# Optimization experiments

Hardware: AMD Instinct MI355X
Metric: run time of the kernel (lower is better)

Reference implementation:

```python
import jax, jax.numpy as jnp
import numpy as np

B, S, D, H = 2, 2048, 1024, 16
ND = D // H  # head dim = 64


def setup_inputs() -> dict:
    key = jax.random.key(0)
    ks = jax.random.split(key, 11)
    scale = 1.0 / np.sqrt(D)
    inp = {
        "q": jax.random.normal(ks[0], (B, S, D), dtype=jnp.float32),
        "k": jax.random.normal(ks[1], (B, S, D), dtype=jnp.float32),
        "v": jax.random.normal(ks[2], (B, S, D), dtype=jnp.float32),
        # causal mask, broadcast over batch and heads
        "mask": jnp.tril(jnp.ones((S, S), dtype=jnp.int32))[None, None, :, :],
        "Wq": jax.random.normal(ks[3], (D, D), dtype=jnp.float32) * scale,
        "bq": jnp.zeros((D,), dtype=jnp.float32),
        "Wk": jax.random.normal(ks[4], (D, D), dtype=jnp.float32) * scale,
        "bk": jnp.zeros((D,), dtype=jnp.float32),
        "Wv": jax.random.normal(ks[5], (D, D), dtype=jnp.float32) * scale,
        "bv": jnp.zeros((D,), dtype=jnp.float32),
        "Wo": jax.random.normal(ks[6], (D, D), dtype=jnp.float32) * scale,
        "bo": jnp.zeros((D,), dtype=jnp.float32),
    }
    return inp


def reference(q, k, v, mask, Wq, bq, Wk, bk, Wv, bv, Wo, bo):
    batch, seq_len, _ = q.shape
    # torch nn.Linear: x @ W.T + b
    qh = (q @ Wq.T + bq).reshape(batch, seq_len, H, ND).transpose(0, 2, 1, 3)
    kh = (k @ Wk.T + bk).reshape(batch, seq_len, H, ND).transpose(0, 2, 1, 3)
    vh = (v @ Wv.T + bv).reshape(batch, seq_len, H, ND).transpose(0, 2, 1, 3)
    # [B,H,S,S] scores
    score = jnp.einsum("bhqd,bhkd->bhqk", qh, kh) / jnp.sqrt(jnp.float32(ND))
    score = jnp.where(mask == 0, jnp.float32(-1e9), score)
    score = jax.nn.softmax(score, axis=-1)
    out = jnp.einsum("bhqk,bhkd->bhqd", score, vh)
    out = out.transpose(0, 2, 1, 3).reshape(batch, seq_len, D)
    return out @ Wo.T + bo
```

## Files before the change

kernel.cpp:

```cpp
#include <hip/hip_runtime.h>
#include <hip/hip_bf16.h>
#include <stdint.h>

#define S_LEN 2048
#define DMODEL 1024
#define NHEAD 16
#define HDIM 64
#define BATCH 2

typedef __bf16 bf16_t;
typedef __attribute__((ext_vector_type(8))) __bf16 bf16x8;
typedef __attribute__((ext_vector_type(4))) __bf16 bf16x4;
typedef __attribute__((ext_vector_type(4))) float f32x4;

#define LOG2E 1.44269504088896340736f

__device__ __forceinline__ void gload_lds16(const void* g, void* l) {
  __builtin_amdgcn_global_load_lds(
      (const __attribute__((address_space(1))) uint32_t*)g,
      (__attribute__((address_space(3))) uint32_t*)l, 16, 0, 0);
}

__global__ __launch_bounds__(256) void convert_all(
    const float* __restrict__ q, const float* __restrict__ k, const float* __restrict__ v,
    const float* __restrict__ wq, const float* __restrict__ wk, const float* __restrict__ wv,
    const float* __restrict__ wo,
    bf16_t* __restrict__ qb, bf16_t* __restrict__ kb, bf16_t* __restrict__ vb,
    bf16_t* __restrict__ wqb, bf16_t* __restrict__ wkb, bf16_t* __restrict__ wvb,
    bf16_t* __restrict__ wob)
{
  const size_t M1 = 1048576;
  size_t e = ((size_t)blockIdx.x * 256 + threadIdx.x) * 4;
  const float* src; bf16_t* dst; size_t off;
  if      (e <  4*M1) { src = q;  dst = qb;  off = e;         }
  else if (e <  8*M1) { src = k;  dst = kb;  off = e - 4*M1;  }
  else if (e < 12*M1) { src = v;  dst = vb;  off = e - 8*M1;  }
  else if (e < 13*M1) { src = wq; dst = wqb; off = e - 12*M1; }
  else if (e < 14*M1) { src = wk; dst = wkb; off = e - 13*M1; }
  else if (e < 15*M1) { src = wv; dst = wvb; off = e - 14*M1; }
  else                { src = wo; dst = wob; off = e - 15*M1; }
  float4 f = *reinterpret_cast<const float4*>(src + off);
  bf16x4 o;
  o[0] = (bf16_t)f.x; o[1] = (bf16_t)f.y; o[2] = (bf16_t)f.z; o[3] = (bf16_t)f.w;
  *reinterpret_cast<bf16x4*>(dst + off) = o;
}

__device__ __forceinline__ void gemm_body(
    const bf16_t* __restrict__ A, const bf16_t* __restrict__ W,
    const float* __restrict__ bias, bf16_t* __restrict__ outb,
    float* __restrict__ outf, int M, int N, int K, float scale, int packmode)
{
  __shared__ bf16_t As[128 * 32];
  __shared__ bf16_t Bs[128 * 32];
  int tid = threadIdx.x;
  int w = tid >> 6, lane = tid & 63;
  int lr = lane & 15, lg = lane >> 4;
  int wr = w >> 1, wc = w & 1;
  int m0 = blockIdx.x * 128, n0 = blockIdx.y * 128;

  f32x4 acc[4][4];
#pragma unroll
  for (int a = 0; a < 4; ++a)
#pragma unroll
    for (int bq = 0; bq < 4; ++bq) acc[a][bq] = (f32x4){0.f, 0.f, 0.f, 0.f};

  int col_st = (lane & 3) * 8;

  for (int kt = 0; kt < K; kt += 32) {
#pragma unroll
    for (int it = 0; it < 2; ++it) {
      int chunkbase = (w * 2 + it) * 512;
      int row = (w * 2 + it) * 16 + (lane >> 2);
      gload_lds16(A + (size_t)(m0 + row) * K + kt + col_st, &As[chunkbase]);
      gload_lds16(W + (size_t)(n0 + row) * K + kt + col_st, &Bs[chunkbase]);
    }
    __syncthreads();
    bf16x8 af[4], bfv[4];
#pragma unroll
    for (int mf = 0; mf < 4; ++mf)
      af[mf] = *reinterpret_cast<const bf16x8*>(&As[(wr * 64 + mf * 16 + lr) * 32 + lg * 8]);
#pragma unroll
    for (int nf = 0; nf < 4; ++nf)
      bfv[nf] = *reinterpret_cast<const bf16x8*>(&Bs[(wc * 64 + nf * 16 + lr) * 32 + lg * 8]);
#pragma unroll
    for (int mf = 0; mf < 4; ++mf)
#pragma unroll
      for (int nf = 0; nf < 4; ++nf)
        acc[mf][nf] = __builtin_amdgcn_mfma_f32_16x16x32_bf16(af[mf], bfv[nf], acc[mf][nf], 0, 0, 0);
    __syncthreads();
  }

#pragma unroll
  for (int mf = 0; mf < 4; ++mf) {
#pragma unroll
    for (int nf = 0; nf < 4; ++nf) {
      int col = n0 + wc * 64 + nf * 16 + lr;
      float bcol = bias[col];
#pragma unroll
      for (int i = 0; i < 4; ++i) {
        int row = m0 + wr * 64 + mf * 16 + lg * 4 + i;
        float vv = (acc[mf][nf][i] + bcol) * scale;
        if (outf) {
          outf[(size_t)row * N + col] = vv;
        } else if (packmode == 0) {
          outb[(size_t)row * N + col] = (bf16_t)vv;
        } else if (packmode == 1) {
          int hh = col >> 6, dh = col & 63;
          int half = dh >> 5, klg = (dh >> 3) & 3, j = dh & 7;
          int bb = row >> 11, s = row & 2047;
          size_t off = ((((size_t)(bb * 16 + hh) * 32 + (s >> 6)) * 4 + ((s >> 4) & 3)) * 2 + half) * 512
                     + (klg * 16 + (s & 15)) * 8 + j;
          outb[off] = (bf16_t)vv;
        } else {
          int hh = col >> 6, d = col & 63;
          int dfo = d >> 4, vlr = d & 15;
          int bb = row >> 11, s = row & 2047;
          int t64 = s >> 6, sin_ = s & 63;
          int half = sin_ >> 5, vlg = (sin_ >> 3) & 3, j = s & 7;
          size_t off = (((size_t)(bb * 16 + hh) * 32 + t64) * 8 + dfo * 2 + half) * 512
                     + (vlg * 16 + vlr) * 8 + j;
          outb[off] = (bf16_t)vv;
        }
      }
    }
  }
}

__global__ __launch_bounds__(256) void gemm_proj(
    const bf16_t* __restrict__ qb, const bf16_t* __restrict__ kb, const bf16_t* __restrict__ vb,
    const bf16_t* __restrict__ wqb, const bf16_t* __restrict__ wkb, const bf16_t* __restrict__ wvb,
    const float* __restrict__ bq, const float* __restrict__ bk, const float* __restrict__ bv,
    bf16_t* __restrict__ Qp, bf16_t* __restrict__ Kpk, bf16_t* __restrict__ Vpk)
{
  int z = blockIdx.z;
  const bf16_t* A = (z == 0) ? qb : (z == 1) ? kb : vb;
  const bf16_t* W = (z == 0) ? wqb : (z == 1) ? wkb : wvb;
  const float* bias = (z == 0) ? bq : (z == 1) ? bk : bv;
  bf16_t* o = (z == 0) ? Qp : (z == 1) ? Kpk : Vpk;
  float scale = (z == 0) ? 0.125f * LOG2E : 1.0f;
  gemm_body(A, W, bias, o, nullptr, BATCH * S_LEN, DMODEL, DMODEL, scale, z);
}

__global__ __launch_bounds__(256) void gemm_out(
    const bf16_t* __restrict__ O, const bf16_t* __restrict__ wob,
    const float* __restrict__ bo, float* __restrict__ out)
{
  gemm_body(O, wob, bo, nullptr, out, BATCH * S_LEN, DMODEL, DMODEL, 1.0f, 0);
}

#define PSTRIDE 66

__global__ __launch_bounds__(512, 4) void attn_fwd(
    const bf16_t* __restrict__ Qp, const bf16_t* __restrict__ Kpk,
    const bf16_t* __restrict__ Vpk, bf16_t* __restrict__ O)
{
  int flat = blockIdx.x;
  int low = flat & 7, kk = flat >> 3;
  int pj = kk & 15;
  int bh = ((kk >> 4) << 3) + low;
  int b = bh >> 4, h = bh & 15;
  int tid = threadIdx.x, wv = tid >> 6, lane = tid & 63;
  int lr = lane & 15, lg = lane >> 4;
  int grp = wv >> 2, wl = wv & 3;
  int qt = grp ? (31 - pj) : pj;

  __shared__ bf16_t Ps[8][16 * PSTRIDE];

  int q_row = qt * 64 + wl * 16 + lr;
  const bf16_t* Qbase = Qp + ((size_t)b * S_LEN + q_row) * DMODEL + h * HDIM + lg * 8;
  bf16x8 qf0 = *reinterpret_cast<const bf16x8*>(Qbase);
  bf16x8 qf1 = *reinterpret_cast<const bf16x8*>(Qbase + 32);

  f32x4 oacc[4];
#pragma unroll
  for (int df = 0; df < 4; ++df) oacc[df] = (f32x4){0.f, 0.f, 0.f, 0.f};
  float m = -1e30f, l = 0.f;

  const bf16_t* Kb = Kpk + (size_t)bh * (32 * 4096) + lane * 8;
  const bf16_t* Vb = Vpk + (size_t)bh * (32 * 4096) + lane * 8;
  bf16_t* ps = &Ps[wv][lr * PSTRIDE];

  bf16x8 kc[8];
  {
    const bf16_t* Kt = Kb;
#pragma unroll
    for (int f = 0; f < 8; ++f) kc[f] = *reinterpret_cast<const bf16x8*>(Kt + f * 512);
  }

  for (int t = 0; t <= qt; ++t) {
    const bf16_t* Vt_ = Vb + t * 4096;

    f32x4 sacc[4];
    __builtin_amdgcn_s_setprio(1);
#pragma unroll
    for (int kvf = 0; kvf < 4; ++kvf) {
      f32x4 s = (f32x4){0.f, 0.f, 0.f, 0.f};
      s = __builtin_amdgcn_mfma_f32_16x16x32_bf16(kc[kvf * 2 + 0], qf0, s, 0, 0, 0);
      s = __builtin_amdgcn_mfma_f32_16x16x32_bf16(kc[kvf * 2 + 1], qf1, s, 0, 0, 0);
      sacc[kvf] = s;
    }
    __builtin_amdgcn_s_setprio(0);

    bf16x8 vf[8];
#pragma unroll
    for (int f = 0; f < 8; ++f)
      vf[f] = *reinterpret_cast<const bf16x8*>(Vt_ + f * 512);

    if (t == qt) {
      int kv0 = t * 64;
#pragma unroll
      for (int kvf = 0; kvf < 4; ++kvf) {
        int kv_g = kv0 + kvf * 16 + lg * 4;
#pragma unroll
        for (int i = 0; i < 4; ++i)
          if (kv_g + i > q_row) sacc[kvf][i] = -1e30f;
      }
    }

    float lmax = fmaxf(fmaxf(sacc[0][0], sacc[0][1]), fmaxf(sacc[0][2], sacc[0][3]));
#pragma unroll
    for (int kvf = 1; kvf < 4; ++kvf)
      lmax = fmaxf(lmax, fmaxf(fmaxf(sacc[kvf][0], sacc[kvf][1]),
                               fmaxf(sacc[kvf][2], sacc[kvf][3])));
    if (__any(lmax > m + 8.f)) {
      float mx = lmax;
      mx = fmaxf(mx, __shfl_xor(mx, 16));
      mx = fmaxf(mx, __shfl_xor(mx, 32));
      float mn = fmaxf(m, mx);
      float rr = __builtin_amdgcn_exp2f(m - mn);
      m = mn; l *= rr;
#pragma unroll
      for (int dfo = 0; dfo < 4; ++dfo) oacc[dfo] *= rr;
    }

    float psum = 0.f;
#pragma unroll
    for (int kvf = 0; kvf < 4; ++kvf) {
      bf16x4 pw;
#pragma unroll
      for (int i = 0; i < 4; ++i) {
        float p = __builtin_amdgcn_exp2f(sacc[kvf][i] - m);
        psum += p;
        pw[i] = (bf16_t)p;
      }
      *reinterpret_cast<bf16x4*>(ps + kvf * 16 + lg * 4) = pw;
    }
    l += psum;

    if (t + 1 <= qt) {
      const bf16_t* Kt = Kb + (t + 1) * 4096;
#pragma unroll
      for (int f = 0; f < 8; ++f) kc[f] = *reinterpret_cast<const bf16x8*>(Kt + f * 512);
    }

    asm volatile("s_waitcnt lgkmcnt(0)" ::: "memory");
    __builtin_amdgcn_sched_barrier(0);

    bf16x8 pa0 = *reinterpret_cast<const bf16x8*>(ps + lg * 8);
    bf16x8 pa1 = *reinterpret_cast<const bf16x8*>(ps + 32 + lg * 8);
    __builtin_amdgcn_s_setprio(1);
#pragma unroll
    for (int dfo = 0; dfo < 4; ++dfo) {
      oacc[dfo] = __builtin_amdgcn_mfma_f32_16x16x32_bf16(vf[dfo * 2 + 0], pa0, oacc[dfo], 0, 0, 0);
      oacc[dfo] = __builtin_amdgcn_mfma_f32_16x16x32_bf16(vf[dfo * 2 + 1], pa1, oacc[dfo], 0, 0, 0);
    }
    __builtin_amdgcn_s_setprio(0);
  }

  l += __shfl_xor(l, 16);
  l += __shfl_xor(l, 32);
  float inv = 1.0f / l;
  bf16_t* ob = O + ((size_t)b * S_LEN + q_row) * DMODEL + h * HDIM + lg * 4;
#pragma unroll
  for (int dfo = 0; dfo < 4; ++dfo) {
    bf16x4 ov;
#pragma unroll
    for (int i = 0; i < 4; ++i) ov[i] = (bf16_t)(oacc[dfo][i] * inv);
    *reinterpret_cast<bf16x4*>(ob + dfo * 16) = ov;
  }
}

extern "C" void kernel_launch(void* const* d_in, const int* in_sizes, int n_in,
                              void* d_out, int out_size, void* d_ws, size_t ws_size,
                              hipStream_t stream) {
  const float* q  = (const float*)d_in[0];
  const float* k  = (const float*)d_in[1];
  const float* v  = (const float*)d_in[2];
  const float* Wq = (const float*)d_in[4];
  const float* bq = (const float*)d_in[5];
  const float* Wk = (const float*)d_in[6];
  const float* bk = (const float*)d_in[7];
  const float* Wv = (const float*)d_in[8];
  const float* bv = (const float*)d_in[9];
  const float* Wo = (const float*)d_in[10];
  const float* bo = (const float*)d_in[11];
  float* out = (float*)d_out;

  const size_t MB = 1u << 20;
  char* base = (char*)d_ws;
  bf16_t* qb  = (bf16_t*)(base + 0 * MB);
  bf16_t* kb  = (bf16_t*)(base + 8 * MB);
  bf16_t* vb  = (bf16_t*)(base + 16 * MB);
  bf16_t* wqb = (bf16_t*)(base + 24 * MB);
  bf16_t* wkb = (bf16_t*)(base + 26 * MB);
  bf16_t* wvb = (bf16_t*)(base + 28 * MB);
  bf16_t* wob = (bf16_t*)(base + 30 * MB);
  bf16_t* Qp  = (bf16_t*)(base + 32 * MB);
  bf16_t* Kpk = (bf16_t*)(base + 40 * MB);
  bf16_t* Vpk = (bf16_t*)(base + 56 * MB);
  bf16_t* Ob  = (bf16_t*)(base + 64 * MB);

  convert_all<<<16384, 256, 0, stream>>>(q, k, v, Wq, Wk, Wv, Wo,
                                         qb, kb, vb, wqb, wkb, wvb, wob);
  gemm_proj<<<dim3(32, 8, 3), 256, 0, stream>>>(qb, kb, vb, wqb, wkb, wvb,
                                                bq, bk, bv, Qp, Kpk, Vpk);
  attn_fwd<<<512, 512, 0, stream>>>(Qp, Kpk, Vpk, Ob);
  gemm_out<<<dim3(32, 8), 256, 0, stream>>>(Ob, wob, bo, out);
}
```

Baseline: 131.1 us.

## Split KV range across wave halves and merge partial softmax via LDS

Each block now handles one query tile instead of a pair, and its two groups of four waves split that tile's KV range in half. The partial max, sum and output are merged through shared memory at the end. The grid doubles to 1024 blocks, launch bounds ask for 8 blocks per CU, and the block-to-tile order is interleaved for load balance. K loads are no longer prefetched one iteration ahead, and the extra shared-memory buffers plus the final __syncthreads add overhead.

```diff
diff --git a/kernel.cpp b/kernel.cpp
--- a/kernel.cpp
+++ b/kernel.cpp
@@ -150,23 +150,30 @@
 
 #define PSTRIDE 66
 
-__global__ __launch_bounds__(512, 4) void attn_fwd(
+__global__ __launch_bounds__(512, 8) void attn_fwd(
     const bf16_t* __restrict__ Qp, const bf16_t* __restrict__ Kpk,
     const bf16_t* __restrict__ Vpk, bf16_t* __restrict__ O)
 {
   int flat = blockIdx.x;
-  int low = flat & 7, kk = flat >> 3;
-  int pj = kk & 15;
-  int bh = ((kk >> 4) << 3) + low;
+  int kblk = flat & 255, rr4 = flat >> 8;
+  int mq = (kblk >> 5) & 7;
+  int bh = kblk & 31;
+  int qt = (rr4 == 0) ? mq : (rr4 == 1) ? 15 - mq : (rr4 == 2) ? 16 + mq : 31 - mq;
   int b = bh >> 4, h = bh & 15;
   int tid = threadIdx.x, wv = tid >> 6, lane = tid & 63;
   int lr = lane & 15, lg = lane >> 4;
-  int grp = wv >> 2, wl = wv & 3;
-  int qt = grp ? (31 - pj) : pj;
+  int sl = wv & 3, hi = wv >> 2;
 
   __shared__ bf16_t Ps[8][16 * PSTRIDE];
-
-  int q_row = qt * 64 + wl * 16 + lr;
+  __shared__ float Ml[4][64];
+  __shared__ float Ll[4][64];
+  __shared__ float Ol[4][64][16];
+
+  int hsp = (qt + 2) >> 1;
+  int t0 = hi ? hsp : 0;
+  int t1 = hi ? qt + 1 : hsp;
+
+  int q_row = qt * 64 + sl * 16 + lr;
   const bf16_t* Qbase = Qp + ((size_t)b * S_LEN + q_row) * DMODEL + h * HDIM + lg * 8;
   bf16x8 qf0 = *reinterpret_cast<const bf16x8*>(Qbase);
   bf16x8 qf1 = *reinterpret_cast<const bf16x8*>(Qbase + 32);
@@ -180,31 +187,29 @@
   const bf16_t* Vb = Vpk + (size_t)bh * (32 * 4096) + lane * 8;
   bf16_t* ps = &Ps[wv][lr * PSTRIDE];
 
-  bf16x8 kc[8];
-  {
-    const bf16_t* Kt = Kb;
-#pragma unroll
-    for (int f = 0; f < 8; ++f) kc[f] = *reinterpret_cast<const bf16x8*>(Kt + f * 512);
-  }
-
-  for (int t = 0; t <= qt; ++t) {
+  for (int t = t0; t < t1; ++t) {
+    const bf16_t* Kt = Kb + t * 4096;
     const bf16_t* Vt_ = Vb + t * 4096;
+
+    bf16x8 kf[8];
+#pragma unroll
+    for (int f = 0; f < 8; ++f)
+      kf[f] = *reinterpret_cast<const bf16x8*>(Kt + f * 512);
+    bf16x8 vf[8];
+#pragma unroll
+    for (int f = 0; f < 8; ++f)
+      vf[f] = *reinterpret_cast<const bf16x8*>(Vt_ + f * 512);
 
     f32x4 sacc[4];
     __builtin_amdgcn_s_setprio(1);
 #pragma unroll
     for (int kvf = 0; kvf < 4; ++kvf) {
       f32x4 s = (f32x4){0.f, 0.f, 0.f, 0.f};
-      s = __builtin_amdgcn_mfma_f32_16x16x32_bf16(kc[kvf * 2 + 0], qf0, s, 0, 0, 0);
-      s = __builtin_amdgcn_mfma_f32_16x16x32_bf16(kc[kvf * 2 + 1], qf1, s, 0, 0, 0);
+      s = __builtin_amdgcn_mfma_f32_16x16x32_bf16(kf[kvf * 2 + 0], qf0, s, 0, 0, 0);
+      s = __builtin_amdgcn_mfma_f32_16x16x32_bf16(kf[kvf * 2 + 1], qf1, s, 0, 0, 0);
       sacc[kvf] = s;
     }
     __builtin_amdgcn_s_setprio(0);
-
-    bf16x8 vf[8];
-#pragma unroll
-    for (int f = 0; f < 8; ++f)
-      vf[f] = *reinterpret_cast<const bf16x8*>(Vt_ + f * 512);
 
     if (t == qt) {
       int kv0 = t * 64;
@@ -227,10 +232,10 @@
       mx = fmaxf(mx, __shfl_xor(mx, 16));
       mx = fmaxf(mx, __shfl_xor(mx, 32));
       float mn = fmaxf(m, mx);
-      float rr = __builtin_amdgcn_exp2f(m - mn);
-      m = mn; l *= rr;
-#pragma unroll
-      for (int dfo = 0; dfo < 4; ++dfo) oacc[dfo] *= rr;
+      float rsc = __builtin_amdgcn_exp2f(m - mn);
+      m = mn; l *= rsc;
+#pragma unroll
+      for (int dfo = 0; dfo < 4; ++dfo) oacc[dfo] *= rsc;
     }
 
     float psum = 0.f;
@@ -247,12 +252,6 @@
     }
     l += psum;
 
-    if (t + 1 <= qt) {
-      const bf16_t* Kt = Kb + (t + 1) * 4096;
-#pragma unroll
-      for (int f = 0; f < 8; ++f) kc[f] = *reinterpret_cast<const bf16x8*>(Kt + f * 512);
-    }
-
     asm volatile("s_waitcnt lgkmcnt(0)" ::: "memory");
     __builtin_amdgcn_sched_barrier(0);
 
@@ -267,16 +266,39 @@
     __builtin_amdgcn_s_setprio(0);
   }
 
-  l += __shfl_xor(l, 16);
-  l += __shfl_xor(l, 32);
-  float inv = 1.0f / l;
-  bf16_t* ob = O + ((size_t)b * S_LEN + q_row) * DMODEL + h * HDIM + lg * 4;
-#pragma unroll
-  for (int dfo = 0; dfo < 4; ++dfo) {
-    bf16x4 ov;
-#pragma unroll
-    for (int i = 0; i < 4; ++i) ov[i] = (bf16_t)(oacc[dfo][i] * inv);
-    *reinterpret_cast<bf16x4*>(ob + dfo * 16) = ov;
+  if (hi) {
+    Ml[sl][lane] = m;
+    Ll[sl][lane] = l;
+#pragma unroll
+    for (int dfo = 0; dfo < 4; ++dfo)
+#pragma unroll
+      for (int i = 0; i < 4; ++i)
+        Ol[sl][lane][dfo * 4 + i] = oacc[dfo][i];
+  }
+  __syncthreads();
+  if (!hi) {
+    float mB = Ml[sl][lane], lB = Ll[sl][lane];
+    float mAB = fmaxf(m, mB);
+    float fA = __builtin_amdgcn_exp2f(m - mAB);
+    float fB = __builtin_amdgcn_exp2f(mB - mAB);
+    l = l * fA + lB * fB;
+#pragma unroll
+    for (int dfo = 0; dfo < 4; ++dfo)
+#pragma unroll
+      for (int i = 0; i < 4; ++i)
+        oacc[dfo][i] = oacc[dfo][i] * fA + Ol[sl][lane][dfo * 4 + i] * fB;
+
+    l += __shfl_xor(l, 16);
+    l += __shfl_xor(l, 32);
+    float inv = 1.0f / l;
+    bf16_t* ob = O + ((size_t)b * S_LEN + q_row) * DMODEL + h * HDIM + lg * 4;
+#pragma unroll
+    for (int dfo = 0; dfo < 4; ++dfo) {
+      bf16x4 ov;
+#pragma unroll
+      for (int i = 0; i < 4; ++i) ov[i] = (bf16_t)(oacc[dfo][i] * inv);
+      *reinterpret_cast<bf16x4*>(ob + dfo * 16) = ov;
+    }
   }
 }
 
@@ -314,6 +336,6 @@
                                          qb, kb, vb, wqb, wkb, wvb, wob);
   gemm_proj<<<dim3(32, 8, 3), 256, 0, stream>>>(qb, kb, vb, wqb, wkb, wvb,
                                                 bq, bk, bv, Qp, Kpk, Vpk);
-  attn_fwd<<<512, 512, 0, stream>>>(Qp, Kpk, Vpk, Ob);
+  attn_fwd<<<1024, 512, 0, stream>>>(Qp, Kpk, Vpk, Ob);
   gemm_out<<<dim3(32, 8), 256, 0, stream>>>(Ob, wob, bo, out);
 }
```

Result: slower. 409.4 us (+212.3%).

## Map attention blocks to contiguous 128-row query tiles with per-wave causal bounds

Applied to the files above, without the earlier changes.

Changes the attention work split from pairing a short and a long 64-row query tile per block (load balancing) to giving each block one contiguous 128-row tile, with each wave stopping at its own causal limit. It adds a block-wide barrier every KV step so waves advance in lockstep, which is meant to let them share K/V tiles through cache. The K register prefetch of the next tile is removed, and K is now loaded together with V at the start of each step. The risks are load imbalance across blocks (later tiles do more work), barrier stalls, and exposed K load latency. The launch grid must still match 16 q-tiles times 32 batch-heads, which holds if the host launches 512 blocks as before.

```diff
diff --git a/kernel.cpp b/kernel.cpp
--- a/kernel.cpp
+++ b/kernel.cpp
@@ -155,18 +155,18 @@
     const bf16_t* __restrict__ Vpk, bf16_t* __restrict__ O)
 {
   int flat = blockIdx.x;
-  int low = flat & 7, kk = flat >> 3;
-  int pj = kk & 15;
-  int bh = ((kk >> 4) << 3) + low;
+  int bh = flat & 31, qt = flat >> 5;
   int b = bh >> 4, h = bh & 15;
   int tid = threadIdx.x, wv = tid >> 6, lane = tid & 63;
   int lr = lane & 15, lg = lane >> 4;
-  int grp = wv >> 2, wl = wv & 3;
-  int qt = grp ? (31 - pj) : pj;
 
   __shared__ bf16_t Ps[8][16 * PSTRIDE];
 
-  int q_row = qt * 64 + wl * 16 + lr;
+  int rbase = qt * 128 + wv * 16;
+  int q_row = rbase + lr;
+  int t_end = (rbase + 15) >> 6;
+  int t_max = (qt * 128 + 127) >> 6;
+
   const bf16_t* Qbase = Qp + ((size_t)b * S_LEN + q_row) * DMODEL + h * HDIM + lg * 8;
   bf16x8 qf0 = *reinterpret_cast<const bf16x8*>(Qbase);
   bf16x8 qf1 = *reinterpret_cast<const bf16x8*>(Qbase + 32);
@@ -180,91 +180,86 @@
   const bf16_t* Vb = Vpk + (size_t)bh * (32 * 4096) + lane * 8;
   bf16_t* ps = &Ps[wv][lr * PSTRIDE];
 
-  bf16x8 kc[8];
-  {
-    const bf16_t* Kt = Kb;
-#pragma unroll
-    for (int f = 0; f < 8; ++f) kc[f] = *reinterpret_cast<const bf16x8*>(Kt + f * 512);
-  }
-
-  for (int t = 0; t <= qt; ++t) {
-    const bf16_t* Vt_ = Vb + t * 4096;
-
-    f32x4 sacc[4];
-    __builtin_amdgcn_s_setprio(1);
-#pragma unroll
-    for (int kvf = 0; kvf < 4; ++kvf) {
-      f32x4 s = (f32x4){0.f, 0.f, 0.f, 0.f};
-      s = __builtin_amdgcn_mfma_f32_16x16x32_bf16(kc[kvf * 2 + 0], qf0, s, 0, 0, 0);
-      s = __builtin_amdgcn_mfma_f32_16x16x32_bf16(kc[kvf * 2 + 1], qf1, s, 0, 0, 0);
-      sacc[kvf] = s;
+  for (int t = 0; t <= t_max; ++t) {
+    if (t <= t_end) {
+      const bf16_t* Kt = Kb + t * 4096;
+      const bf16_t* Vt_ = Vb + t * 4096;
+
+      bf16x8 kf[8];
+#pragma unroll
+      for (int f = 0; f < 8; ++f)
+        kf[f] = *reinterpret_cast<const bf16x8*>(Kt + f * 512);
+      bf16x8 vf[8];
+#pragma unroll
+      for (int f = 0; f < 8; ++f)
+        vf[f] = *reinterpret_cast<const bf16x8*>(Vt_ + f * 512);
+
+      f32x4 sacc[4];
+      __builtin_amdgcn_s_setprio(1);
+#pragma unroll
+      for (int kvf = 0; kvf < 4; ++kvf) {
+        f32x4 s = (f32x4){0.f, 0.f, 0.f, 0.f};
+        s = __builtin_amdgcn_mfma_f32_16x16x32_bf16(kf[kvf * 2 + 0], qf0, s, 0, 0, 0);
+        s = __builtin_amdgcn_mfma_f32_16x16x32_bf16(kf[kvf * 2 + 1], qf1, s, 0, 0, 0);
+        sacc[kvf] = s;
+      }
+      __builtin_amdgcn_s_setprio(0);
+
+      if (t == t_end) {
+        int kv0 = t * 64;
+#pragma unroll
+        for (int kvf = 0; kvf < 4; ++kvf) {
+          int kv_g = kv0 + kvf * 16 + lg * 4;
+#pragma unroll
+          for (int i = 0; i < 4; ++i)
+            if (kv_g + i > q_row) sacc[kvf][i] = -1e30f;
+        }
+      }
+
+      float lmax = fmaxf(fmaxf(sacc[0][0], sacc[0][1]), fmaxf(sacc[0][2], sacc[0][3]));
+#pragma unroll
+      for (int kvf = 1; kvf < 4; ++kvf)
+        lmax = fmaxf(lmax, fmaxf(fmaxf(sacc[kvf][0], sacc[kvf][1]),
+                                 fmaxf(sacc[kvf][2], sacc[kvf][3])));
+      if (__any(lmax > m + 8.f)) {
+        float mx = lmax;
+        mx = fmaxf(mx, __shfl_xor(mx, 16));
+        mx = fmaxf(mx, __shfl_xor(mx, 32));
+        float mn = fmaxf(m, mx);
+        float rsc = __builtin_amdgcn_exp2f(m - mn);
+        m = mn; l *= rsc;
+#pragma unroll
+        for (int dfo = 0; dfo < 4; ++dfo) oacc[dfo] *= rsc;
+      }
+
+      float psum = 0.f;
+#pragma unroll
+      for (int kvf = 0; kvf < 4; ++kvf) {
+        bf16x4 pw;
+#pragma unroll
+        for (int i = 0; i < 4; ++i) {
+          float p = __builtin_amdgcn_exp2f(sacc[kvf][i] - m);
+          psum += p;
+          pw[i] = (bf16_t)p;
+        }
+        *reinterpret_cast<bf16x4*>(ps + kvf * 16 + lg * 4) = pw;
+      }
+      l += psum;
+
+      asm volatile("s_waitcnt lgkmcnt(0)" ::: "memory");
+      __builtin_amdgcn_sched_barrier(0);
+
+      bf16x8 pa0 = *reinterpret_cast<const bf16x8*>(ps + lg * 8);
+      bf16x8 pa1 = *reinterpret_cast<const bf16x8*>(ps + 32 + lg * 8);
+      __builtin_amdgcn_s_setprio(1);
+#pragma unroll
+      for (int dfo = 0; dfo < 4; ++dfo) {
+        oacc[dfo] = __builtin_amdgcn_mfma_f32_16x16x32_bf16(vf[dfo * 2 + 0], pa0, oacc[dfo], 0, 0, 0);
+        oacc[dfo] = __builtin_amdgcn_mfma_f32_16x16x32_bf16(vf[dfo * 2 + 1], pa1, oacc[dfo], 0, 0, 0);
+      }
+      __builtin_amdgcn_s_setprio(0);
     }
-    __builtin_amdgcn_s_setprio(0);
-
-    bf16x8 vf[8];
-#pragma unroll
-    for (int f = 0; f < 8; ++f)
-      vf[f] = *reinterpret_cast<const bf16x8*>(Vt_ + f * 512);
-
-    if (t == qt) {
-      int kv0 = t * 64;
-#pragma unroll
-      for (int kvf = 0; kvf < 4; ++kvf) {
-        int kv_g = kv0 + kvf * 16 + lg * 4;
-#pragma unroll
-        for (int i = 0; i < 4; ++i)
-          if (kv_g + i > q_row) sacc[kvf][i] = -1e30f;
-      }
-    }
-
-    float lmax = fmaxf(fmaxf(sacc[0][0], sacc[0][1]), fmaxf(sacc[0][2], sacc[0][3]));
-#pragma unroll
-    for (int kvf = 1; kvf < 4; ++kvf)
-      lmax = fmaxf(lmax, fmaxf(fmaxf(sacc[kvf][0], sacc[kvf][1]),
-                               fmaxf(sacc[kvf][2], sacc[kvf][3])));
-    if (__any(lmax > m + 8.f)) {
-      float mx = lmax;
-      mx = fmaxf(mx, __shfl_xor(mx, 16));
-      mx = fmaxf(mx, __shfl_xor(mx, 32));
-      float mn = fmaxf(m, mx);
-      float rr = __builtin_amdgcn_exp2f(m - mn);
-      m = mn; l *= rr;
-#pragma unroll
-      for (int dfo = 0; dfo < 4; ++dfo) oacc[dfo] *= rr;
-    }
-
-    float psum = 0.f;
-#pragma unroll
-    for (int kvf = 0; kvf < 4; ++kvf) {
-      bf16x4 pw;
-#pragma unroll
-      for (int i = 0; i < 4; ++i) {
-        float p = __builtin_amdgcn_exp2f(sacc[kvf][i] - m);
-        psum += p;
-        pw[i] = (bf16_t)p;
-      }
-      *reinterpret_cast<bf16x4*>(ps + kvf * 16 + lg * 4) = pw;
-    }
-    l += psum;
-
-    if (t + 1 <= qt) {
-      const bf16_t* Kt = Kb + (t + 1) * 4096;
-#pragma unroll
-      for (int f = 0; f < 8; ++f) kc[f] = *reinterpret_cast<const bf16x8*>(Kt + f * 512);
-    }
-
-    asm volatile("s_waitcnt lgkmcnt(0)" ::: "memory");
-    __builtin_amdgcn_sched_barrier(0);
-
-    bf16x8 pa0 = *reinterpret_cast<const bf16x8*>(ps + lg * 8);
-    bf16x8 pa1 = *reinterpret_cast<const bf16x8*>(ps + 32 + lg * 8);
-    __builtin_amdgcn_s_setprio(1);
-#pragma unroll
-    for (int dfo = 0; dfo < 4; ++dfo) {
-      oacc[dfo] = __builtin_amdgcn_mfma_f32_16x16x32_bf16(vf[dfo * 2 + 0], pa0, oacc[dfo], 0, 0, 0);
-      oacc[dfo] = __builtin_amdgcn_mfma_f32_16x16x32_bf16(vf[dfo * 2 + 1], pa1, oacc[dfo], 0, 0, 0);
-    }
-    __builtin_amdgcn_s_setprio(0);
+    __builtin_amdgcn_s_barrier();
   }
 
   l += __shfl_xor(l, 16);
```

Measured after the change: 166.9 us. 1.27x slower.
